# Kernel tuning notes

Hardware: AMD Instinct MI355X
Metric: run time of the kernel (lower is better)

## Reference

```python
import jax, jax.numpy as jnp
import numpy as np

HIDDEN = 4096
NUM_HEADS = 32
HEAD_DIM = 128
NUM_KV_HEADS = 8
KV_GROUPS = NUM_HEADS // NUM_KV_HEADS
ROPE_THETA = 10000.0
SEQ = 2048
BATCH = 1
NEG_INF = -1e9


def fake_quant_int8(x):
    """Per-tensor symmetric int8 fake quantization (absmax scale)."""
    scale = jnp.maximum(jnp.max(jnp.abs(x)) / 127.0, 1e-8)
    q = jnp.clip(jnp.round(x / scale), -127.0, 127.0) * scale
    # straight-through estimator (no-op in fwd-only, keeps code shared)
    return x + jax.lax.stop_gradient(q - x)


def rotate_half(x):
    x1, x2 = jnp.split(x, 2, axis=-1)
    return jnp.concatenate([-x2, x1], axis=-1)


def rope_cos_sin(position_ids):
    inv_freq = 1.0 / (ROPE_THETA ** (jnp.arange(0, HEAD_DIM, 2, dtype=jnp.float32) / HEAD_DIM))
    freqs = position_ids.astype(jnp.float32)[..., None] * inv_freq  # [B,S,HD/2]
    emb = jnp.concatenate([freqs, freqs], axis=-1)                  # [B,S,HD]
    return jnp.cos(emb), jnp.sin(emb)


def setup_inputs() -> dict:
    key = jax.random.key(0)
    k1, k2, k3, k4, k5 = jax.random.split(key, 5)
    hidden_states = jax.random.normal(k1, (BATCH, SEQ, HIDDEN), dtype=jnp.float32)
    causal = jnp.tril(jnp.ones((SEQ, SEQ), dtype=bool))
    attention_mask = jnp.where(causal, 0.0, NEG_INF).astype(jnp.float32)[None, None]  # [1,1,S,S]
    position_ids = jnp.arange(SEQ, dtype=jnp.int64 if jax.config.jax_enable_x64 else jnp.int32)[None, :]
    s = 0.02
    wq = jax.random.normal(k2, (NUM_HEADS * HEAD_DIM, HIDDEN), dtype=jnp.float32) * s
    wk = jax.random.normal(k3, (NUM_KV_HEADS * HEAD_DIM, HIDDEN), dtype=jnp.float32) * s
    wv = jax.random.normal(k4, (NUM_KV_HEADS * HEAD_DIM, HIDDEN), dtype=jnp.float32) * s
    wo = jax.random.normal(k5, (HIDDEN, NUM_HEADS * HEAD_DIM), dtype=jnp.float32) * s
    return {"hidden_states": hidden_states, "attention_mask": attention_mask,
            "position_ids": position_ids, "wq": wq, "wk": wk, "wv": wv, "wo": wo}


def reference(hidden_states, attention_mask, position_ids, wq, wk, wv, wo):
    B, S, _ = hidden_states.shape

    def qlinear(x, w):  # quantized linear: fake-quant act and weight, y = x @ w.T
        return fake_quant_int8(x) @ fake_quant_int8(w).T

    q = qlinear(hidden_states, wq).reshape(B, S, NUM_HEADS, HEAD_DIM).transpose(0, 2, 1, 3)
    k = qlinear(hidden_states, wk).reshape(B, S, NUM_KV_HEADS, HEAD_DIM).transpose(0, 2, 1, 3)
    v = qlinear(hidden_states, wv).reshape(B, S, NUM_KV_HEADS, HEAD_DIM).transpose(0, 2, 1, 3)

    cos, sin = rope_cos_sin(position_ids)      # [B,S,HD]
    cos, sin = cos[:, None], sin[:, None]      # [B,1,S,HD]
    q = q * cos + rotate_half(q) * sin
    k = k * cos + rotate_half(k) * sin

    # repeat_kv: GQA -> full heads
    k = jnp.repeat(k, KV_GROUPS, axis=1)
    v = jnp.repeat(v, KV_GROUPS, axis=1)

    # quantized QK^T
    scores = jnp.einsum('bhqd,bhkd->bhqk', fake_quant_int8(q), fake_quant_int8(k))
    scores = scores * (1.0 / np.sqrt(HEAD_DIM).astype(np.float32))
    scores = scores + attention_mask[:, :, :, :S]
    probs = jax.nn.softmax(scores.astype(jnp.float32), axis=-1).astype(q.dtype)
    # attention_dropout = 0.0 -> identity

    # quantized AV
    attn_out = jnp.einsum('bhqk,bhkd->bhqd', fake_quant_int8(probs), fake_quant_int8(v))
    attn_out = attn_out.transpose(0, 2, 1, 3).reshape(B, S, NUM_HEADS * HEAD_DIM)
    return qlinear(attn_out, wo)
```

## Files before the change

kernel.cpp:

```cpp
#include <hip/hip_runtime.h>
#include <stdint.h>

#define SEQ   2048
#define HID   4096
#define NH    32
#define NKV   8
#define KVDIM 1024
#define KVCAT 2048

typedef int v4i __attribute__((ext_vector_type(4)));

#define VMCNT0 asm volatile("s_waitcnt vmcnt(0)" ::: "memory")

__device__ __forceinline__ void gload16(const void* g, void* l) {
    __builtin_amdgcn_global_load_lds(
        (const __attribute__((address_space(1))) void*)(uintptr_t)g,
        (__attribute__((address_space(3))) void*)(uintptr_t)l, 16, 0, 0);
}

__device__ __forceinline__ float slot_scale(const unsigned* slots, int slot) {
    return fmaxf(__uint_as_float(slots[slot << 5]) / 127.0f, 1e-8f);
}

__device__ __forceinline__ int q8v(float x, float s) {
    int v = (int)rintf(x / s);
    return v < -127 ? -127 : (v > 127 ? 127 : v);
}

__device__ __forceinline__ float fexp2(float x) {
    float r; asm("v_exp_f32 %0, %1" : "=v"(r) : "v"(x)); return r;
}

__device__ __forceinline__ float amax4(const float* __restrict__ p, long v) {
    float4 x = *(const float4*)(p + v * 4);
    return fmaxf(fmaxf(fabsf(x.x), fabsf(x.y)), fmaxf(fabsf(x.z), fabsf(x.w)));
}

__device__ __forceinline__ void block_amax_store(float m, float* part) {
    __shared__ float sm[4];
    int lane = threadIdx.x & 63, w = threadIdx.x >> 6;
    for (int off = 32; off; off >>= 1) m = fmaxf(m, __shfl_xor(m, off, 64));
    if (lane == 0) sm[w] = m;
    __syncthreads();
    if (threadIdx.x == 0)
        part[blockIdx.x] = fmaxf(fmaxf(sm[0], sm[1]), fmaxf(sm[2], sm[3]));
}

#define NV0 ((long)SEQ * HID / 4)
#define NV1 ((long)HID * HID / 4)
#define NV2 ((long)KVDIM * HID / 4)
__global__ void k_absmax5(const float* __restrict__ a0, const float* __restrict__ a1,
                          const float* __restrict__ a2, const float* __restrict__ a3,
                          const float* __restrict__ a4, float* __restrict__ part) {
    int b = blockIdx.x;
    const float* p; long n; int lb, nb;
    if (b < 342)       { p = a0; n = NV0; lb = b;        nb = 342; }
    else if (b < 1025) { p = a1; n = NV1; lb = b - 342;  nb = 683; }
    else if (b < 1196) { p = a2; n = NV2; lb = b - 1025; nb = 171; }
    else if (b < 1367) { p = a3; n = NV2; lb = b - 1196; nb = 171; }
    else               { p = a4; n = NV1; lb = b - 1367; nb = 681; }
    long str = (long)nb * 256;
    float mm[8] = {0.f, 0.f, 0.f, 0.f, 0.f, 0.f, 0.f, 0.f};
    long v = (long)lb * 256 + threadIdx.x;
    for (; v + 7 * str < n; v += 8 * str) {
        #pragma unroll
        for (int j = 0; j < 8; j++) mm[j] = fmaxf(mm[j], amax4(p, v + j * str));
    }
    for (; v < n; v += str) mm[0] = fmaxf(mm[0], amax4(p, v));
    float m = fmaxf(fmaxf(fmaxf(mm[0], mm[1]), fmaxf(mm[2], mm[3])),
                    fmaxf(fmaxf(mm[4], mm[5]), fmaxf(mm[6], mm[7])));
    block_amax_store(m, part);
}

__global__ void k_reduceA(const float* __restrict__ part, unsigned* slots) {
    __shared__ float sm[4];
    const int lo[5] = {0, 342, 1025, 1196, 1367};
    const int hi[5] = {342, 1025, 1196, 1367, 2048};
    int t = threadIdx.x, lane = t & 63, w = t >> 6;
    for (int s = 0; s < 5; s++) {
        float m = 0.f;
        for (int i = lo[s] + t; i < hi[s]; i += 256) m = fmaxf(m, part[i]);
        for (int off = 32; off; off >>= 1) m = fmaxf(m, __shfl_xor(m, off, 64));
        if (lane == 0) sm[w] = m;
        __syncthreads();
        if (t == 0)
            slots[s << 5] = __float_as_uint(fmaxf(fmaxf(sm[0], sm[1]), fmaxf(sm[2], sm[3])));
        __syncthreads();
    }
}

__global__ void k_reduceB(const float* __restrict__ p1, const float* __restrict__ p2,
                          const float* __restrict__ p3, unsigned* slots) {
    __shared__ float sm[4];
    int t = threadIdx.x, lane = t & 63, w = t >> 6;
    const float* ps[3] = {p1, p2, p3};
    const int cnt[3] = {2048, 1024, 256};
    const int sl[3] = {5, 6, 7};
    for (int s = 0; s < 3; s++) {
        float m = 0.f;
        for (int i = t; i < cnt[s]; i += 256) m = fmaxf(m, ps[s][i]);
        for (int off = 32; off; off >>= 1) m = fmaxf(m, __shfl_xor(m, off, 64));
        if (lane == 0) sm[w] = m;
        __syncthreads();
        if (t == 0)
            slots[sl[s] << 5] = __float_as_uint(fmaxf(fmaxf(sm[0], sm[1]), fmaxf(sm[2], sm[3])));
        __syncthreads();
    }
}

__device__ __forceinline__ void qstore4(const float* __restrict__ src, long v,
                                        int8_t* __restrict__ dst, float s) {
    float4 x = *(const float4*)(src + v * 4);
    unsigned pa = (unsigned)(uint8_t)(int8_t)q8v(x.x, s)
                | ((unsigned)(uint8_t)(int8_t)q8v(x.y, s) << 8)
                | ((unsigned)(uint8_t)(int8_t)q8v(x.z, s) << 16)
                | ((unsigned)(uint8_t)(int8_t)q8v(x.w, s) << 24);
    *(unsigned*)(dst + v * 4) = pa;
}

__global__ void k_quant4(const float* __restrict__ a0, const float* __restrict__ a1,
                         const float* __restrict__ a2, const float* __restrict__ a3,
                         int8_t* __restrict__ d0, int8_t* __restrict__ d1,
                         int8_t* __restrict__ d2, int8_t* __restrict__ d3,
                         const unsigned* __restrict__ slots) {
    int b = blockIdx.x;
    const float* p; int8_t* d; long n; int slot, lb, nb;
    if (b < 512)       { p = a0; d = d0; n = NV0; slot = 0; lb = b;        nb = 512; }
    else if (b < 1536) { p = a1; d = d1; n = NV1; slot = 1; lb = b - 512;  nb = 1024; }
    else if (b < 1792) { p = a2; d = d2; n = NV2; slot = 2; lb = b - 1536; nb = 256; }
    else               { p = a3; d = d3; n = NV2; slot = 3; lb = b - 1792; nb = 256; }
    float s = slot_scale(slots, slot);
    long str = (long)nb * 256;
    long v = (long)lb * 256 + threadIdx.x;
    for (; v + 3 * str < n; v += 4 * str) {
        #pragma unroll
        for (int j = 0; j < 4; j++) qstore4(p, v + j * str, d, s);
    }
    for (; v < n; v += str) qstore4(p, v, d, s);
}

__global__ void k_quant(const float* __restrict__ x, int8_t* __restrict__ q, long nvec,
                        int rshift, long cmaskv, long ld,
                        const unsigned* __restrict__ slots, int slot) {
    float s = slot_scale(slots, slot);
    long gs = (long)gridDim.x * blockDim.x;
    long v = blockIdx.x * (long)blockDim.x + threadIdx.x;
    for (; v + 3 * gs < nvec; v += 4 * gs) {
        #pragma unroll
        for (int j = 0; j < 4; j++) {
            long vid = v + j * gs;
            long r = vid >> rshift;
            long c = (vid & cmaskv) << 2;
            float4 vv = *(const float4*)(x + r * ld + c);
            unsigned pa = (unsigned)(uint8_t)(int8_t)q8v(vv.x, s)
                        | ((unsigned)(uint8_t)(int8_t)q8v(vv.y, s) << 8)
                        | ((unsigned)(uint8_t)(int8_t)q8v(vv.z, s) << 16)
                        | ((unsigned)(uint8_t)(int8_t)q8v(vv.w, s) << 24);
            *(unsigned*)(q + vid * 4) = pa;
        }
    }
    for (; v < nvec; v += gs) {
        long r = v >> rshift;
        long c = (v & cmaskv) << 2;
        float4 vv = *(const float4*)(x + r * ld + c);
        unsigned pa = (unsigned)(uint8_t)(int8_t)q8v(vv.x, s)
                    | ((unsigned)(uint8_t)(int8_t)q8v(vv.y, s) << 8)
                    | ((unsigned)(uint8_t)(int8_t)q8v(vv.z, s) << 16)
                    | ((unsigned)(uint8_t)(int8_t)q8v(vv.w, s) << 24);
        *(unsigned*)(q + v * 4) = pa;
    }
}

__global__ void k_ropetab(const int* __restrict__ pos, float* __restrict__ ct,
                          float* __restrict__ st) {
    int tid = blockIdx.x * blockDim.x + threadIdx.x;
    if (tid >= SEQ * 64) return;
    int i = tid & 63, s = tid >> 6;
    double inv = 1.0 / pow(10000.0, (double)((float)(2 * i) * (1.0f / 128.0f)));
    float invf = (float)inv;
    float angf = (float)pos[s] * invf;
    double a = (double)angf;
    ct[tid] = (float)cos(a);
    st[tid] = (float)sin(a);
}

__global__ void k_rope(float* __restrict__ x, long ld, int hbits, int total,
                       const float* __restrict__ ct, const float* __restrict__ st,
                       float* __restrict__ part) {
    float m = 0.f;
    for (int t = blockIdx.x * blockDim.x + threadIdx.x; t < total;
         t += gridDim.x * blockDim.x) {
        int i4 = t & 15;
        int h = (t >> 4) & ((1 << hbits) - 1);
        int s = t >> (4 + hbits);
        long base = (long)s * ld + h * 128 + i4 * 4;
        float4 a = *(float4*)(x + base);
        float4 b = *(float4*)(x + base + 64);
        float4 c = *(const float4*)(ct + s * 64 + i4 * 4);
        float4 sn = *(const float4*)(st + s * 64 + i4 * 4);
        float4 o0, o1;
        o0.x = a.x * c.x - b.x * sn.x;  o1.x = b.x * c.x + a.x * sn.x;
        o0.y = a.y * c.y - b.y * sn.y;  o1.y = b.y * c.y + a.y * sn.y;
        o0.z = a.z * c.z - b.z * sn.z;  o1.z = b.z * c.z + a.z * sn.z;
        o0.w = a.w * c.w - b.w * sn.w;  o1.w = b.w * c.w + a.w * sn.w;
        *(float4*)(x + base) = o0;
        *(float4*)(x + base + 64) = o1;
        m = fmaxf(m,
            fmaxf(fmaxf(fmaxf(fabsf(o0.x), fabsf(o0.y)), fmaxf(fabsf(o0.z), fabsf(o0.w))),
                  fmaxf(fmaxf(fabsf(o1.x), fabsf(o1.y)), fmaxf(fabsf(o1.z), fabsf(o1.w)))));
    }
    block_amax_store(m, part);
}

__global__ void k_transq(const float* __restrict__ src, long lds_, int8_t* __restrict__ dst,
                         long ldd, const unsigned* __restrict__ slots, int slot) {
    __shared__ float t[32][33];
    float s = slot_scale(slots, slot);
    int bx = blockIdx.x, by = blockIdx.y;
    int tid = threadIdx.x;
    int c = tid & 31, r0 = tid >> 5;
    #pragma unroll
    for (int j = 0; j < 4; j++) {
        int r = r0 + j * 8;
        t[r][c] = src[(long)(by * 32 + r) * lds_ + bx * 32 + c];
    }
    __syncthreads();
    int d = tid >> 3, k4 = (tid & 7) * 4;
    unsigned pa = 0;
    #pragma unroll
    for (int j = 0; j < 4; j++) {
        int iv = q8v(t[k4 + j][d], s);
        pa |= ((unsigned)(uint8_t)(int8_t)iv) << (8 * j);
    }
    *(unsigned*)(dst + (long)(bx * 32 + d) * ldd + by * 32 + k4) = pa;
}

__global__ __launch_bounds__(256) void k_gemm_i8(
    const int8_t* __restrict__ A, const int8_t* __restrict__ B, float* __restrict__ C,
    int M, int N, int K, unsigned* slots,
    int slotA, int slotB, int slotB2, int nsplit, float* am_part, int am_col0) {
    __shared__ int8_t As[2][128 * 128];
    __shared__ int8_t Bs[2][128 * 128];
    const v4i vzero = {0, 0, 0, 0};
    int tid = threadIdx.x, lane = tid & 63, wid = tid >> 6;
    int nbx = N >> 7;
    int nwg = gridDim.x, wg = blockIdx.x;
    int cpx = nwg >> 3;
    int swz = (wg & 7) * cpx + (wg >> 3);
    int bm = swz / nbx, bn = swz % nbx;
    long rowA0 = (long)bm * 128, colB0 = (long)bn * 128;
    int wrow = (wid >> 1) * 64, wcol = (wid & 1) * 64;
    int lr = lane >> 3;
    int swc = ((lane & 7) ^ lr) * 16;
    const int8_t* ga = A + (rowA0 + wid * 8 + lr) * (long)K + swc;
    const int8_t* gb = B + (colB0 + wid * 8 + lr) * (long)K + swc;
    v4i acc[4][4];
    #pragma unroll
    for (int m = 0; m < 4; m++)
        #pragma unroll
        for (int n = 0; n < 4; n++) acc[m][n] = vzero;

    auto STAGE = [&](int buf, int kt) {
        #pragma unroll
        for (int i = 0; i < 4; i++) {
            gload16(ga + kt + (long)(i * 32) * K, &As[buf][(wid * 8 + i * 32) * 128]);
            gload16(gb + kt + (long)(i * 32) * K, &Bs[buf][(wid * 8 + i * 32) * 128]);
        }
    };
    auto COMPUTE = [&](int buf) {
        #pragma unroll
        for (int ks = 0; ks < 2; ks++) {
            v4i af[4], bf[4];
            #pragma unroll
            for (int m = 0; m < 4; m++) {
                int row = wrow + m * 16 + (lane & 15);
                af[m] = *(const v4i*)(&As[buf][row * 128 + (((ks * 4 + (lane >> 4)) ^ (row & 7)) * 16)]);
            }
            #pragma unroll
            for (int n = 0; n < 4; n++) {
                int row = wcol + n * 16 + (lane & 15);
                bf[n] = *(const v4i*)(&Bs[buf][row * 128 + (((ks * 4 + (lane >> 4)) ^ (row & 7)) * 16)]);
            }
            #pragma unroll
            for (int m = 0; m < 4; m++)
                #pragma unroll
                for (int n = 0; n < 4; n++)
                    acc[m][n] = __builtin_amdgcn_mfma_i32_16x16x64_i8(af[m], bf[n], acc[m][n], 0, 0, 0);
        }
    };

    STAGE(0, 0);
    VMCNT0;
    __syncthreads();
    int nt = K >> 7, cur = 0;
    for (int t = 0; t < nt - 1; t++) {
        STAGE(cur ^ 1, (t + 1) << 7);
        COMPUTE(cur);
        VMCNT0;
        __syncthreads();
        cur ^= 1;
    }
    COMPUTE(cur);

    float sA = slot_scale(slots, slotA);
    float sB1 = slot_scale(slots, slotB);
    float sB2 = slot_scale(slots, slotB2);
    float am = 0.f;
    #pragma unroll
    for (int m = 0; m < 4; m++) {
        long row0 = rowA0 + wrow + m * 16 + ((lane >> 4) << 2);
        #pragma unroll
        for (int n = 0; n < 4; n++) {
            int col = (int)colB0 + wcol + n * 16 + (lane & 15);
            float sc = sA * ((col < nsplit) ? sB1 : sB2);
            float* cp = C + row0 * N + col;
            #pragma unroll
            for (int r = 0; r < 4; r++) {
                float val = sc * (float)acc[m][n][r];
                cp[(long)r * N] = val;
                if (col >= am_col0) am = fmaxf(am, fabsf(val));
            }
        }
    }
    if (am_part) block_amax_store(am, am_part);
}

__global__ __launch_bounds__(256) void k_attn(
    const int8_t* __restrict__ Qq, const int8_t* __restrict__ Kq, const int8_t* __restrict__ Vtq,
    int* __restrict__ AO, unsigned* slots) {
    __shared__ int8_t Qs[64 * 128];
    __shared__ int8_t Ks[2][64 * 128];
    __shared__ int8_t Vs[2][128 * 64];
    __shared__ int smx[4];
    const v4i vzero = {0, 0, 0, 0};
    const int NEGS = -(1 << 29);
    int tid = threadIdx.x, lane = tid & 63, w = tid >> 6;
    int qlan = lane & 15, g = lane >> 4;
    int idx = blockIdx.x;
    int qb = 31 - (idx >> 5), h = idx & 31, kvh = h >> 2;
    float sq = slot_scale(slots, 5), sk = slot_scale(slots, 6);
    float c2 = sq * sk * 0.08838834764831845f * 1.4426950408889634f;
    int lr8 = lane >> 3;
    int swc = ((lane & 7) ^ lr8) * 16;
    int lr4 = lane >> 2;
    int vswc = ((lane & 3) ^ (lr4 & 3)) * 16;
    const int8_t* kbase = Kq + ((long)(w * 8 + lr8)) * KVDIM + kvh * 128 + swc;
    const int8_t* vbase = Vtq + ((long)kvh * 128 + w * 16 + lr4) * SEQ + vswc;
    auto STAGE_K = [&](int buf, int kt) {
        #pragma unroll
        for (int i = 0; i < 2; i++)
            gload16(kbase + ((long)kt * 64 + i * 32) * KVDIM, &Ks[buf][(w * 8 + i * 32) * 128]);
    };
    auto STAGE_V = [&](int buf, int kt) {
        #pragma unroll
        for (int i = 0; i < 2; i++)
            gload16(vbase + (long)(i * 64) * SEQ + kt * 64, &Vs[buf][(w * 16 + i * 64) * 64]);
    };
    {
        const int8_t* qbase = Qq + ((long)qb * 64 + w * 8 + lr8) * HID + h * 128 + swc;
        #pragma unroll
        for (int i = 0; i < 2; i++)
            gload16(qbase + (long)(i * 32) * HID, &Qs[(w * 8 + i * 32) * 128]);
    }
    STAGE_K(0, 0);
    VMCNT0;
    __syncthreads();
    v4i aq[2];
    #pragma unroll
    for (int ks = 0; ks < 2; ks++) {
        int row = w * 16 + qlan;
        aq[ks] = *(const v4i*)(&Qs[row * 128 + (((ks * 4 + g) ^ (row & 7)) * 16)]);
    }
    int mi = -(1 << 30);
    float l = 0.f;
    int buf = 0;
    for (int kt = 0; kt <= qb; kt++) {
        if (kt < qb) STAGE_K(buf ^ 1, kt + 1);
        v4i sf[4] = {vzero, vzero, vzero, vzero};
        __builtin_amdgcn_s_setprio(1);
        #pragma unroll
        for (int ks = 0; ks < 2; ks++)
            #pragma unroll
            for (int f = 0; f < 4; f++) {
                int row = f * 16 + qlan;
                v4i bk = *(const v4i*)(&Ks[buf][row * 128 + (((ks * 4 + g) ^ (row & 7)) * 16)]);
                sf[f] = __builtin_amdgcn_mfma_i32_16x16x64_i8(bk, aq[ks], sf[f], 0, 0, 0);
            }
        __builtin_amdgcn_s_setprio(0);
        int sv[16];
        if (kt == qb) {
            int qthr = w * 16 + qlan;
            #pragma unroll
            for (int f = 0; f < 4; f++)
                #pragma unroll
                for (int r = 0; r < 4; r++) {
                    int kl = f * 16 + g * 4 + r;
                    sv[f * 4 + r] = (kl > qthr) ? NEGS : sf[f][r];
                }
        } else {
            #pragma unroll
            for (int f = 0; f < 4; f++)
                #pragma unroll
                for (int r = 0; r < 4; r++) sv[f * 4 + r] = sf[f][r];
        }
        int tm = sv[0];
        #pragma unroll
        for (int e = 1; e < 16; e++) tm = tm > sv[e] ? tm : sv[e];
        tm = max(tm, __shfl_xor(tm, 16, 64));
        tm = max(tm, __shfl_xor(tm, 32, 64));
        int mn = tm > mi ? tm : mi;
        float esc = fexp2(c2 * (float)(mi - mn));
        float es = 0.f;
        #pragma unroll
        for (int e = 0; e < 16; e++) es += fexp2(c2 * (float)(sv[e] - mn));
        es += __shfl_xor(es, 16, 64);
        es += __shfl_xor(es, 32, 64);
        l = l * esc + es;
        mi = mn;
        VMCNT0;
        __syncthreads();
        buf ^= 1;
    }
    float invl = 127.0f / l;
    unsigned* Ps32 = (unsigned*)Qs;
    int pwr = w * 320;
    v4i of[8];
    #pragma unroll
    for (int nf = 0; nf < 8; nf++) of[nf] = vzero;
    STAGE_K(0, 0);
    STAGE_V(0, 0);
    VMCNT0;
    __syncthreads();
    buf = 0;
    for (int kt = 0; kt <= qb; kt++) {
        if (kt < qb) { STAGE_K(buf ^ 1, kt + 1); STAGE_V(buf ^ 1, kt + 1); }
        v4i sf[4] = {vzero, vzero, vzero, vzero};
        __builtin_amdgcn_s_setprio(1);
        #pragma unroll
        for (int ks = 0; ks < 2; ks++)
            #pragma unroll
            for (int f = 0; f < 4; f++) {
                int row = f * 16 + qlan;
                v4i bk = *(const v4i*)(&Ks[buf][row * 128 + (((ks * 4 + g) ^ (row & 7)) * 16)]);
                sf[f] = __builtin_amdgcn_mfma_i32_16x16x64_i8(bk, aq[ks], sf[f], 0, 0, 0);
            }
        __builtin_amdgcn_s_setprio(0);
        if (kt == qb) {
            int qthr = w * 16 + qlan;
            #pragma unroll
            for (int f = 0; f < 4; f++) {
                unsigned pk = 0;
                #pragma unroll
                for (int r = 0; r < 4; r++) {
                    int kl = f * 16 + g * 4 + r;
                    int s = (kl > qthr) ? NEGS : sf[f][r];
                    float t = fexp2(c2 * (float)(s - mi));
                    int pq = (int)rintf(t * invl);
                    pk |= ((unsigned)pq) << (8 * r);
                }
                Ps32[pwr + (4 * f + g) * 20 + qlan] = pk;
            }
        } else {
            #pragma unroll
            for (int f = 0; f < 4; f++) {
                unsigned pk = 0;
                #pragma unroll
                for (int r = 0; r < 4; r++) {
                    float t = fexp2(c2 * (float)(sf[f][r] - mi));
                    int pq = (int)rintf(t * invl);
                    pk |= ((unsigned)pq) << (8 * r);
                }
                Ps32[pwr + (4 * f + g) * 20 + qlan] = pk;
            }
        }
        int rb = pwr + 80 * g + qlan;
        v4i ap;
        ap[0] = (int)Ps32[rb];
        ap[1] = (int)Ps32[rb + 20];
        ap[2] = (int)Ps32[rb + 40];
        ap[3] = (int)Ps32[rb + 60];
        __builtin_amdgcn_s_setprio(1);
        #pragma unroll
        for (int nf = 0; nf < 8; nf++) {
            int row = nf * 16 + qlan;
            v4i bv = *(const v4i*)(&Vs[buf][row * 64 + ((g ^ (row & 3)) * 16)]);
            of[nf] = __builtin_amdgcn_mfma_i32_16x16x64_i8(ap, bv, of[nf], 0, 0, 0);
        }
        __builtin_amdgcn_s_setprio(0);
        VMCNT0;
        __syncthreads();
        buf ^= 1;
    }
    int mymax = 0;
    #pragma unroll
    for (int nf = 0; nf < 8; nf++)
        #pragma unroll
        for (int r = 0; r < 4; r++) {
            int val = of[nf][r];
            int av = val < 0 ? -val : val;
            mymax = av > mymax ? av : mymax;
            int qg = qb * 64 + w * 16 + 4 * g + r;
            AO[(long)qg * HID + h * 128 + nf * 16 + qlan] = val;
        }
    #pragma unroll
    for (int off = 1; off < 64; off <<= 1) {
        int o2 = __shfl_xor(mymax, off, 64);
        mymax = o2 > mymax ? o2 : mymax;
    }
    if (lane == 0) smx[w] = mymax;
    __syncthreads();
    if (tid == 0) {
        int mm = max(max(smx[0], smx[1]), max(smx[2], smx[3]));
        atomicMax(slots + (8 << 5), (unsigned)mm);
    }
}

__global__ void k_quant_ao(const int* __restrict__ a, int8_t* __restrict__ q, unsigned* slots) {
    float sv = slot_scale(slots, 7);
    float spv = (1.0f / 127.0f) * sv;
    float amax = spv * (float)(int)slots[8 << 5];
    float s = fmaxf(amax / 127.0f, 1e-8f);
    long nvec = (long)SEQ * HID / 4;
    long gs = (long)gridDim.x * blockDim.x;
    long v = blockIdx.x * (long)blockDim.x + threadIdx.x;
    for (; v + 3 * gs < nvec; v += 4 * gs) {
        #pragma unroll
        for (int j = 0; j < 4; j++) {
            long vid = v + j * gs;
            int4 x = *(const int4*)(a + vid * 4);
            int a0 = q8v(spv * (float)x.x, s);
            int a1 = q8v(spv * (float)x.y, s);
            int a2 = q8v(spv * (float)x.z, s);
            int a3 = q8v(spv * (float)x.w, s);
            unsigned pa = (unsigned)(uint8_t)(int8_t)a0
                        | ((unsigned)(uint8_t)(int8_t)a1 << 8)
                        | ((unsigned)(uint8_t)(int8_t)a2 << 16)
                        | ((unsigned)(uint8_t)(int8_t)a3 << 24);
            *(unsigned*)(q + vid * 4) = pa;
        }
    }
    for (; v < nvec; v += gs) {
        int4 x = *(const int4*)(a + v * 4);
        int a0 = q8v(spv * (float)x.x, s);
        int a1 = q8v(spv * (float)x.y, s);
        int a2 = q8v(spv * (float)x.z, s);
        int a3 = q8v(spv * (float)x.w, s);
        unsigned pa = (unsigned)(uint8_t)(int8_t)a0
                    | ((unsigned)(uint8_t)(int8_t)a1 << 8)
                    | ((unsigned)(uint8_t)(int8_t)a2 << 16)
                    | ((unsigned)(uint8_t)(int8_t)a3 << 24);
        *(unsigned*)(q + v * 4) = pa;
    }
    if (blockIdx.x == 0 && threadIdx.x == 0) slots[9 << 5] = __float_as_uint(amax);
}

extern "C" void kernel_launch(void* const* d_in, const int* in_sizes, int n_in,
                              void* d_out, int out_size, void* d_ws, size_t ws_size,
                              hipStream_t stream) {
    (void)in_sizes; (void)n_in; (void)out_size;
    const float* hid = (const float*)d_in[0];
    const int* pos = (const int*)d_in[2];
    const float* wqp = (const float*)d_in[3];
    const float* wkp = (const float*)d_in[4];
    const float* wvp = (const float*)d_in[5];
    const float* wop = (const float*)d_in[6];
    float* out = (float*)d_out;
    char* ws = (char*)d_ws;

    size_t o = 0;
    auto alloc = [&](size_t sz) { size_t r = o; o += (sz + 255) & ~(size_t)255; return r; };
    unsigned* slots = (unsigned*)(ws + alloc(2048));
    float* P0 = (float*)(ws + alloc(2048 * 4));
    float* P1 = (float*)(ws + alloc(2048 * 4));
    float* P2 = (float*)(ws + alloc(1024 * 4));
    float* P3 = (float*)(ws + alloc(256 * 4));
    int8_t* Xq   = (int8_t*)(ws + alloc((size_t)SEQ * HID));
    int8_t* Wqq  = (int8_t*)(ws + alloc((size_t)HID * HID));
    int8_t* Wkvq = (int8_t*)(ws + alloc((size_t)KVCAT * HID));
    float*  Qf   = (float*)(ws + alloc((size_t)SEQ * HID * 4));
    float*  KVf  = (float*)(ws + alloc((size_t)SEQ * KVCAT * 4));
    int8_t* Qq   = (int8_t*)(ws + alloc((size_t)SEQ * HID));
    int8_t* Kq   = (int8_t*)(ws + alloc((size_t)SEQ * KVDIM));
    int8_t* Vtq  = (int8_t*)(ws + alloc((size_t)KVDIM * SEQ));
    float*  ctab = (float*)(ws + alloc((size_t)SEQ * 64 * 4));
    float*  stab = (float*)(ws + alloc((size_t)SEQ * 64 * 4));
    if (ws_size < o) return;
    int8_t* Woq = Wqq;
    int*    AOint = (int*)Qf;
    int8_t* AOq = Xq;

    hipMemsetAsync(slots, 0, 2048, stream);
    k_ropetab<<<SEQ * 64 / 256, 256, 0, stream>>>(pos, ctab, stab);
    k_absmax5<<<2048, 256, 0, stream>>>(hid, wqp, wkp, wvp, wop, P0);
    k_reduceA<<<1, 256, 0, stream>>>(P0, slots);
    k_quant4<<<2048, 256, 0, stream>>>(hid, wqp, wkp, wvp,
                                       Xq, Wqq, Wkvq, Wkvq + (size_t)KVDIM * HID, slots);
    k_gemm_i8<<<512, 256, 0, stream>>>(Xq, Wqq, Qf, SEQ, HID, HID, slots,
                                       0, 1, 1, 1 << 30, nullptr, 1 << 30);
    k_gemm_i8<<<256, 256, 0, stream>>>(Xq, Wkvq, KVf, SEQ, KVCAT, HID, slots,
                                       0, 2, 3, KVDIM, P3, KVDIM);
    const long CALL = 0x3FFFFFFFL;
    k_quant<<<2048, 256, 0, stream>>>(wop, Woq, (long)HID * HID / 4, 40, CALL, 0, slots, 4);
    k_rope<<<2048, 256, 0, stream>>>(Qf, HID, 5, SEQ * NH * 16, ctab, stab, P1);
    k_rope<<<1024, 256, 0, stream>>>(KVf, KVCAT, 3, SEQ * NKV * 16, ctab, stab, P2);
    k_reduceB<<<1, 256, 0, stream>>>(P1, P2, P3, slots);
    k_quant<<<2048, 256, 0, stream>>>(Qf, Qq, (long)SEQ * HID / 4, 40, CALL, 0, slots, 5);
    k_quant<<<512, 256, 0, stream>>>(KVf, Kq, (long)SEQ * KVDIM / 4, 8, 255, KVCAT, slots, 6);
    k_transq<<<dim3(32, 64), 256, 0, stream>>>(KVf + KVDIM, KVCAT, Vtq, SEQ, slots, 7);
    k_attn<<<1024, 256, 0, stream>>>(Qq, Kq, Vtq, AOint, slots);
    k_quant_ao<<<2048, 256, 0, stream>>>(AOint, AOq, slots);
    k_gemm_i8<<<512, 256, 0, stream>>>(AOq, Woq, out, SEQ, HID, HID, slots,
                                       9, 4, 4, 1 << 30, nullptr, 1 << 30);
}
```

Measured before the change: 312.6 us.

## Fuse RoPE and absmax into GEMM epilogues, add 256x128 GEMM tile, simplify softmax quant

Result: no change. 309.8 us (-0.9%).

```diff
diff --git a/kernel.cpp b/kernel.cpp
--- a/kernel.cpp
+++ b/kernel.cpp
@@ -36,14 +36,30 @@
     return fmaxf(fmaxf(fabsf(x.x), fabsf(x.y)), fmaxf(fabsf(x.z), fabsf(x.w)));
 }
 
-__device__ __forceinline__ void block_amax_store(float m, float* part) {
+__device__ __forceinline__ void block_amax_part(float m, float* dst) {
     __shared__ float sm[4];
     int lane = threadIdx.x & 63, w = threadIdx.x >> 6;
     for (int off = 32; off; off >>= 1) m = fmaxf(m, __shfl_xor(m, off, 64));
     if (lane == 0) sm[w] = m;
     __syncthreads();
     if (threadIdx.x == 0)
-        part[blockIdx.x] = fmaxf(fmaxf(sm[0], sm[1]), fmaxf(sm[2], sm[3]));
+        *dst = fmaxf(fmaxf(sm[0], sm[1]), fmaxf(sm[2], sm[3]));
+    __syncthreads();
+}
+
+__device__ __forceinline__ void block_amax_part8(float m, float* dst) {
+    __shared__ float sm8[8];
+    int lane = threadIdx.x & 63, w = threadIdx.x >> 6;
+    for (int off = 32; off; off >>= 1) m = fmaxf(m, __shfl_xor(m, off, 64));
+    if (lane == 0) sm8[w] = m;
+    __syncthreads();
+    if (threadIdx.x == 0) {
+        float r = sm8[0];
+        #pragma unroll
+        for (int i = 1; i < 8; i++) r = fmaxf(r, sm8[i]);
+        *dst = r;
+    }
+    __syncthreads();
 }
 
 #define NV0 ((long)SEQ * HID / 4)
@@ -69,7 +85,7 @@
     for (; v < n; v += str) mm[0] = fmaxf(mm[0], amax4(p, v));
     float m = fmaxf(fmaxf(fmaxf(mm[0], mm[1]), fmaxf(mm[2], mm[3])),
                     fmaxf(fmaxf(mm[4], mm[5]), fmaxf(mm[6], mm[7])));
-    block_amax_store(m, part);
+    block_amax_part(m, part + blockIdx.x);
 }
 
 __global__ void k_reduceA(const float* __restrict__ part, unsigned* slots) {
@@ -94,7 +110,7 @@
     __shared__ float sm[4];
     int t = threadIdx.x, lane = t & 63, w = t >> 6;
     const float* ps[3] = {p1, p2, p3};
-    const int cnt[3] = {2048, 1024, 256};
+    const int cnt[3] = {256, 128, 128};
     const int sl[3] = {5, 6, 7};
     for (int s = 0; s < 3; s++) {
         float m = 0.f;
@@ -184,34 +200,6 @@
     st[tid] = (float)sin(a);
 }
 
-__global__ void k_rope(float* __restrict__ x, long ld, int hbits, int total,
-                       const float* __restrict__ ct, const float* __restrict__ st,
-                       float* __restrict__ part) {
-    float m = 0.f;
-    for (int t = blockIdx.x * blockDim.x + threadIdx.x; t < total;
-         t += gridDim.x * blockDim.x) {
-        int i4 = t & 15;
-        int h = (t >> 4) & ((1 << hbits) - 1);
-        int s = t >> (4 + hbits);
-        long base = (long)s * ld + h * 128 + i4 * 4;
-        float4 a = *(float4*)(x + base);
-        float4 b = *(float4*)(x + base + 64);
-        float4 c = *(const float4*)(ct + s * 64 + i4 * 4);
-        float4 sn = *(const float4*)(st + s * 64 + i4 * 4);
-        float4 o0, o1;
-        o0.x = a.x * c.x - b.x * sn.x;  o1.x = b.x * c.x + a.x * sn.x;
-        o0.y = a.y * c.y - b.y * sn.y;  o1.y = b.y * c.y + a.y * sn.y;
-        o0.z = a.z * c.z - b.z * sn.z;  o1.z = b.z * c.z + a.z * sn.z;
-        o0.w = a.w * c.w - b.w * sn.w;  o1.w = b.w * c.w + a.w * sn.w;
-        *(float4*)(x + base) = o0;
-        *(float4*)(x + base + 64) = o1;
-        m = fmaxf(m,
-            fmaxf(fmaxf(fmaxf(fabsf(o0.x), fabsf(o0.y)), fmaxf(fabsf(o0.z), fabsf(o0.w))),
-                  fmaxf(fmaxf(fabsf(o1.x), fabsf(o1.y)), fmaxf(fabsf(o1.z), fabsf(o1.w)))));
-    }
-    block_amax_store(m, part);
-}
-
 __global__ void k_transq(const float* __restrict__ src, long lds_, int8_t* __restrict__ dst,
                          long ldd, const unsigned* __restrict__ slots, int slot) {
     __shared__ float t[32][33];
@@ -238,9 +226,12 @@
 __global__ __launch_bounds__(256) void k_gemm_i8(
     const int8_t* __restrict__ A, const int8_t* __restrict__ B, float* __restrict__ C,
     int M, int N, int K, unsigned* slots,
-    int slotA, int slotB, int slotB2, int nsplit, float* am_part, int am_col0) {
-    __shared__ int8_t As[2][128 * 128];
-    __shared__ int8_t Bs[2][128 * 128];
+    int slotA, int slotB, int slotB2, int nsplit,
+    float* pK, float* pV,
+    const float* __restrict__ ct, const float* __restrict__ st) {
+    __shared__ int8_t POOL[65536];
+    int8_t (*As)[16384] = (int8_t(*)[16384])POOL;
+    int8_t (*Bs)[16384] = (int8_t(*)[16384])(POOL + 32768);
     const v4i vzero = {0, 0, 0, 0};
     int tid = threadIdx.x, lane = tid & 63, wid = tid >> 6;
     int nbx = N >> 7;
@@ -305,24 +296,195 @@
     float sA = slot_scale(slots, slotA);
     float sB1 = slot_scale(slots, slotB);
     float sB2 = slot_scale(slots, slotB2);
-    float am = 0.f;
+    int qc = lane & 15, rgrp = (lane >> 4) << 2;
+    if (bn < 8) {
+        __syncthreads();
+        float* EX = (float*)POOL;
+        #pragma unroll
+        for (int m = 0; m < 4; m++)
+            #pragma unroll
+            for (int n = 0; n < 4; n++) {
+                int coll = wcol + n * 16 + qc;
+                #pragma unroll
+                for (int r = 0; r < 4; r++) {
+                    int rowl = wrow + m * 16 + rgrp + r;
+                    EX[rowl * 128 + (coll ^ ((rowl & 1) << 4))] = sA * sB1 * (float)acc[m][n][r];
+                }
+            }
+        __syncthreads();
+        float am = 0.f;
+        #pragma unroll
+        for (int m = 0; m < 4; m++)
+            #pragma unroll
+            for (int n = 0; n < 4; n++) {
+                int coll = wcol + n * 16 + qc;
+                #pragma unroll
+                for (int r = 0; r < 4; r++) {
+                    int rowl = wrow + m * 16 + rgrp + r;
+                    long srow = rowA0 + rowl;
+                    float self = EX[rowl * 128 + (coll ^ ((rowl & 1) << 4))];
+                    float pv = EX[rowl * 128 + ((coll ^ 64) ^ ((rowl & 1) << 4))];
+                    float c = ct[srow * 64 + (coll & 63)];
+                    float sn = st[srow * 64 + (coll & 63)];
+                    float o = (coll < 64) ? self * c - pv * sn : self * c + pv * sn;
+                    am = fmaxf(am, fabsf(o));
+                    C[srow * N + colB0 + coll] = o;
+                }
+            }
+        block_amax_part(am, pK + bm * 8 + (bn & 7));
+    } else {
+        float am = 0.f;
+        #pragma unroll
+        for (int m = 0; m < 4; m++) {
+            long row0 = rowA0 + wrow + m * 16 + rgrp;
+            #pragma unroll
+            for (int n = 0; n < 4; n++) {
+                int col = (int)colB0 + wcol + n * 16 + qc;
+                float sc = sA * ((col < nsplit) ? sB1 : sB2);
+                float* cp = C + row0 * N + col;
+                #pragma unroll
+                for (int r = 0; r < 4; r++) {
+                    float val = sc * (float)acc[m][n][r];
+                    cp[(long)r * N] = val;
+                    am = fmaxf(am, fabsf(val));
+                }
+            }
+        }
+        block_amax_part(am, pV + bm * 8 + (bn & 7));
+    }
+}
+
+__global__ __launch_bounds__(512) void k_gemm_big(
+    const int8_t* __restrict__ A, const int8_t* __restrict__ B, float* __restrict__ C,
+    int N, int K, unsigned* slots, int slotA, int slotB,
+    float* pQ, int do_rope,
+    const float* __restrict__ ct, const float* __restrict__ st) {
+    __shared__ int8_t POOL[98304];
+    int8_t (*As)[32768] = (int8_t(*)[32768])POOL;
+    int8_t (*Bs)[16384] = (int8_t(*)[16384])(POOL + 65536);
+    const v4i vzero = {0, 0, 0, 0};
+    int tid = threadIdx.x, lane = tid & 63, wid = tid >> 6;
+    int nbx = N >> 7;
+    int nwg = gridDim.x, wg = blockIdx.x;
+    int cpx = nwg >> 3;
+    int swz = (wg & 7) * cpx + (wg >> 3);
+    int bm = swz / nbx, bn = swz % nbx;
+    long rowA0 = (long)bm * 256, colB0 = (long)bn * 128;
+    int wrow = (wid >> 1) * 64, wcol = (wid & 1) * 64;
+    int lr = lane >> 3;
+    int swc = ((lane & 7) ^ lr) * 16;
+    const int8_t* ga = A + (rowA0 + wid * 8 + lr) * (long)K + swc;
+    const int8_t* gb = B + (colB0 + wid * 8 + lr) * (long)K + swc;
+    v4i acc[4][4];
     #pragma unroll
-    for (int m = 0; m < 4; m++) {
-        long row0 = rowA0 + wrow + m * 16 + ((lane >> 4) << 2);
-        #pragma unroll
-        for (int n = 0; n < 4; n++) {
-            int col = (int)colB0 + wcol + n * 16 + (lane & 15);
-            float sc = sA * ((col < nsplit) ? sB1 : sB2);
-            float* cp = C + row0 * N + col;
-            #pragma unroll
-            for (int r = 0; r < 4; r++) {
-                float val = sc * (float)acc[m][n][r];
-                cp[(long)r * N] = val;
-                if (col >= am_col0) am = fmaxf(am, fabsf(val));
-            }
-        }
-    }
-    if (am_part) block_amax_store(am, am_part);
+    for (int m = 0; m < 4; m++)
+        #pragma unroll
+        for (int n = 0; n < 4; n++) acc[m][n] = vzero;
+
+    auto STAGE = [&](int buf, int kt) {
+        #pragma unroll
+        for (int i = 0; i < 4; i++)
+            gload16(ga + kt + (long)(i * 64) * K, &As[buf][(wid * 8 + i * 64) * 128]);
+        #pragma unroll
+        for (int i = 0; i < 2; i++)
+            gload16(gb + kt + (long)(i * 64) * K, &Bs[buf][(wid * 8 + i * 64) * 128]);
+    };
+    auto COMPUTE = [&](int buf) {
+        #pragma unroll
+        for (int ks = 0; ks < 2; ks++) {
+            v4i af[4], bf[4];
+            #pragma unroll
+            for (int m = 0; m < 4; m++) {
+                int row = wrow + m * 16 + (lane & 15);
+                af[m] = *(const v4i*)(&As[buf][row * 128 + (((ks * 4 + (lane >> 4)) ^ (row & 7)) * 16)]);
+            }
+            #pragma unroll
+            for (int n = 0; n < 4; n++) {
+                int row = wcol + n * 16 + (lane & 15);
+                bf[n] = *(const v4i*)(&Bs[buf][row * 128 + (((ks * 4 + (lane >> 4)) ^ (row & 7)) * 16)]);
+            }
+            #pragma unroll
+            for (int m = 0; m < 4; m++)
+                #pragma unroll
+                for (int n = 0; n < 4; n++)
+                    acc[m][n] = __builtin_amdgcn_mfma_i32_16x16x64_i8(af[m], bf[n], acc[m][n], 0, 0, 0);
+        }
+    };
+
+    STAGE(0, 0);
+    VMCNT0;
+    __syncthreads();
+    int nt = K >> 7, cur = 0;
+    for (int t = 0; t < nt - 1; t++) {
+        STAGE(cur ^ 1, (t + 1) << 7);
+        COMPUTE(cur);
+        VMCNT0;
+        __syncthreads();
+        cur ^= 1;
+    }
+    COMPUTE(cur);
+
+    float sA = slot_scale(slots, slotA);
+    float sB1 = slot_scale(slots, slotB);
+    int qc = lane & 15, rgrp = (lane >> 4) << 2;
+    if (do_rope) {
+        float am = 0.f;
+        float* EX = (float*)POOL;
+        __syncthreads();
+        #pragma unroll
+        for (int half = 0; half < 2; half++) {
+            if ((wid >> 2) == half) {
+                #pragma unroll
+                for (int m = 0; m < 4; m++)
+                    #pragma unroll
+                    for (int n = 0; n < 4; n++) {
+                        int coll = wcol + n * 16 + qc;
+                        #pragma unroll
+                        for (int r = 0; r < 4; r++) {
+                            int exr = wrow + m * 16 + rgrp + r - half * 128;
+                            EX[exr * 128 + (coll ^ (((exr >> 2) & 3) << 4))] =
+                                sA * sB1 * (float)acc[m][n][r];
+                        }
+                    }
+            }
+            __syncthreads();
+            if ((wid >> 2) == half) {
+                #pragma unroll
+                for (int m = 0; m < 4; m++)
+                    #pragma unroll
+                    for (int n = 0; n < 4; n++) {
+                        int coll = wcol + n * 16 + qc;
+                        #pragma unroll
+                        for (int r = 0; r < 4; r++) {
+                            int exr = wrow + m * 16 + rgrp + r - half * 128;
+                            int xm = ((exr >> 2) & 3) << 4;
+                            float self = EX[exr * 128 + (coll ^ xm)];
+                            float pv = EX[exr * 128 + ((coll ^ 64) ^ xm)];
+                            long srow = rowA0 + half * 128 + exr;
+                            float c = ct[srow * 64 + (coll & 63)];
+                            float sn = st[srow * 64 + (coll & 63)];
+                            float o = (coll < 64) ? self * c - pv * sn : self * c + pv * sn;
+                            am = fmaxf(am, fabsf(o));
+                            C[srow * N + colB0 + coll] = o;
+                        }
+                    }
+            }
+            __syncthreads();
+        }
+        block_amax_part8(am, pQ + blockIdx.x);
+    } else {
+        #pragma unroll
+        for (int m = 0; m < 4; m++) {
+            long row0 = rowA0 + wrow + m * 16 + rgrp;
+            #pragma unroll
+            for (int n = 0; n < 4; n++) {
+                int col = (int)colB0 + wcol + n * 16 + qc;
+                float* cp = C + row0 * N + col;
+                #pragma unroll
+                for (int r = 0; r < 4; r++) cp[(long)r * N] = sA * sB1 * (float)acc[m][n][r];
+            }
+        }
+    }
 }
 
 __global__ __launch_bounds__(256) void k_attn(
@@ -334,6 +496,7 @@
     __shared__ int smx[4];
     const v4i vzero = {0, 0, 0, 0};
     const int NEGS = -(1 << 29);
+    const float MAGIC = 12582912.0f;
     int tid = threadIdx.x, lane = tid & 63, w = tid >> 6;
     int qlan = lane & 15, g = lane >> 4;
     int idx = blockIdx.x;
@@ -409,10 +572,12 @@
         tm = max(tm, __shfl_xor(tm, 16, 64));
         tm = max(tm, __shfl_xor(tm, 32, 64));
         int mn = tm > mi ? tm : mi;
-        float esc = fexp2(c2 * (float)(mi - mn));
+        float fm = (float)mn;
+        float nb = -c2 * fm;
+        float esc = fexp2(fmaf((float)mi, c2, nb));
         float es = 0.f;
         #pragma unroll
-        for (int e = 0; e < 16; e++) es += fexp2(c2 * (float)(sv[e] - mn));
+        for (int e = 0; e < 16; e++) es += fexp2(fmaf((float)sv[e], c2, nb));
         es += __shfl_xor(es, 16, 64);
         es += __shfl_xor(es, 32, 64);
         l = l * esc + es;
@@ -421,7 +586,7 @@
         __syncthreads();
         buf ^= 1;
     }
-    float invl = 127.0f / l;
+    float Bq = fmaf(c2, (float)mi, __log2f(l) - 6.9886846867721655f);
     unsigned* Ps32 = (unsigned*)Qs;
     int pwr = w * 320;
     v4i of[8];
@@ -454,9 +619,9 @@
                 for (int r = 0; r < 4; r++) {
                     int kl = f * 16 + g * 4 + r;
                     int s = (kl > qthr) ? NEGS : sf[f][r];
-                    float t = fexp2(c2 * (float)(s - mi));
-                    int pq = (int)rintf(t * invl);
-                    pk |= ((unsigned)pq) << (8 * r);
+                    float t = fexp2(fmaf((float)s, c2, -Bq));
+                    unsigned u = __float_as_uint(t + MAGIC) & 127u;
+                    pk |= u << (8 * r);
                 }
                 Ps32[pwr + (4 * f + g) * 20 + qlan] = pk;
             }
@@ -466,9 +631,9 @@
                 unsigned pk = 0;
                 #pragma unroll
                 for (int r = 0; r < 4; r++) {
-                    float t = fexp2(c2 * (float)(sf[f][r] - mi));
-                    int pq = (int)rintf(t * invl);
-                    pk |= ((unsigned)pq) << (8 * r);
+                    float t = fexp2(fmaf((float)sf[f][r], c2, -Bq));
+                    unsigned u = __float_as_uint(t + MAGIC) & 127u;
+                    pk |= u << (8 * r);
                 }
                 Ps32[pwr + (4 * f + g) * 20 + qlan] = pk;
             }
@@ -571,9 +736,9 @@
     auto alloc = [&](size_t sz) { size_t r = o; o += (sz + 255) & ~(size_t)255; return r; };
     unsigned* slots = (unsigned*)(ws + alloc(2048));
     float* P0 = (float*)(ws + alloc(2048 * 4));
-    float* P1 = (float*)(ws + alloc(2048 * 4));
-    float* P2 = (float*)(ws + alloc(1024 * 4));
-    float* P3 = (float*)(ws + alloc(256 * 4));
+    float* P1 = (float*)(ws + alloc(256 * 4));
+    float* P2 = (float*)(ws + alloc(128 * 4));
+    float* P3 = (float*)(ws + alloc(128 * 4));
     int8_t* Xq   = (int8_t*)(ws + alloc((size_t)SEQ * HID));
     int8_t* Wqq  = (int8_t*)(ws + alloc((size_t)HID * HID));
     int8_t* Wkvq = (int8_t*)(ws + alloc((size_t)KVCAT * HID));
@@ -595,20 +760,18 @@
     k_reduceA<<<1, 256, 0, stream>>>(P0, slots);
     k_quant4<<<2048, 256, 0, stream>>>(hid, wqp, wkp, wvp,
                                        Xq, Wqq, Wkvq, Wkvq + (size_t)KVDIM * HID, slots);
-    k_gemm_i8<<<512, 256, 0, stream>>>(Xq, Wqq, Qf, SEQ, HID, HID, slots,
-                                       0, 1, 1, 1 << 30, nullptr, 1 << 30);
+    k_gemm_big<<<256, 512, 0, stream>>>(Xq, Wqq, Qf, HID, HID, slots,
+                                        0, 1, P1, 1, ctab, stab);
     k_gemm_i8<<<256, 256, 0, stream>>>(Xq, Wkvq, KVf, SEQ, KVCAT, HID, slots,
-                                       0, 2, 3, KVDIM, P3, KVDIM);
+                                       0, 2, 3, KVDIM, P2, P3, ctab, stab);
     const long CALL = 0x3FFFFFFFL;
     k_quant<<<2048, 256, 0, stream>>>(wop, Woq, (long)HID * HID / 4, 40, CALL, 0, slots, 4);
-    k_rope<<<2048, 256, 0, stream>>>(Qf, HID, 5, SEQ * NH * 16, ctab, stab, P1);
-    k_rope<<<1024, 256, 0, stream>>>(KVf, KVCAT, 3, SEQ * NKV * 16, ctab, stab, P2);
     k_reduceB<<<1, 256, 0, stream>>>(P1, P2, P3, slots);
     k_quant<<<2048, 256, 0, stream>>>(Qf, Qq, (long)SEQ * HID / 4, 40, CALL, 0, slots, 5);
     k_quant<<<512, 256, 0, stream>>>(KVf, Kq, (long)SEQ * KVDIM / 4, 8, 255, KVCAT, slots, 6);
     k_transq<<<dim3(32, 64), 256, 0, stream>>>(KVf + KVDIM, KVCAT, Vtq, SEQ, slots, 7);
     k_attn<<<1024, 256, 0, stream>>>(Qq, Kq, Vtq, AOint, slots);
     k_quant_ao<<<2048, 256, 0, stream>>>(AOint, AOq, slots);
-    k_gemm_i8<<<512, 256, 0, stream>>>(AOq, Woq, out, SEQ, HID, HID, slots,
-                                       9, 4, 4, 1 << 30, nullptr, 1 << 30);
-}
+    k_gemm_big<<<256, 512, 0, stream>>>(AOq, Woq, out, HID, HID, slots,
+                                        9, 4, nullptr, 0, nullptr, nullptr);
+}
```

## Fuse RoPE and absmax into int8 GEMM epilogue; cheapen softmax quantization

Applied to the files above, without the earlier changes.

After: 301.0 us. -3.7%, faster.

```diff
diff --git a/kernel.cpp b/kernel.cpp
--- a/kernel.cpp
+++ b/kernel.cpp
@@ -36,14 +36,15 @@
     return fmaxf(fmaxf(fabsf(x.x), fabsf(x.y)), fmaxf(fabsf(x.z), fabsf(x.w)));
 }
 
-__device__ __forceinline__ void block_amax_store(float m, float* part) {
+__device__ __forceinline__ void block_amax_part(float m, float* dst) {
     __shared__ float sm[4];
     int lane = threadIdx.x & 63, w = threadIdx.x >> 6;
     for (int off = 32; off; off >>= 1) m = fmaxf(m, __shfl_xor(m, off, 64));
     if (lane == 0) sm[w] = m;
     __syncthreads();
     if (threadIdx.x == 0)
-        part[blockIdx.x] = fmaxf(fmaxf(sm[0], sm[1]), fmaxf(sm[2], sm[3]));
+        *dst = fmaxf(fmaxf(sm[0], sm[1]), fmaxf(sm[2], sm[3]));
+    __syncthreads();
 }
 
 #define NV0 ((long)SEQ * HID / 4)
@@ -69,7 +70,7 @@
     for (; v < n; v += str) mm[0] = fmaxf(mm[0], amax4(p, v));
     float m = fmaxf(fmaxf(fmaxf(mm[0], mm[1]), fmaxf(mm[2], mm[3])),
                     fmaxf(fmaxf(mm[4], mm[5]), fmaxf(mm[6], mm[7])));
-    block_amax_store(m, part);
+    block_amax_part(m, part + blockIdx.x);
 }
 
 __global__ void k_reduceA(const float* __restrict__ part, unsigned* slots) {
@@ -94,7 +95,7 @@
     __shared__ float sm[4];
     int t = threadIdx.x, lane = t & 63, w = t >> 6;
     const float* ps[3] = {p1, p2, p3};
-    const int cnt[3] = {2048, 1024, 256};
+    const int cnt[3] = {512, 128, 128};
     const int sl[3] = {5, 6, 7};
     for (int s = 0; s < 3; s++) {
         float m = 0.f;
@@ -184,34 +185,6 @@
     st[tid] = (float)sin(a);
 }
 
-__global__ void k_rope(float* __restrict__ x, long ld, int hbits, int total,
-                       const float* __restrict__ ct, const float* __restrict__ st,
-                       float* __restrict__ part) {
-    float m = 0.f;
-    for (int t = blockIdx.x * blockDim.x + threadIdx.x; t < total;
-         t += gridDim.x * blockDim.x) {
-        int i4 = t & 15;
-        int h = (t >> 4) & ((1 << hbits) - 1);
-        int s = t >> (4 + hbits);
-        long base = (long)s * ld + h * 128 + i4 * 4;
-        float4 a = *(float4*)(x + base);
-        float4 b = *(float4*)(x + base + 64);
-        float4 c = *(const float4*)(ct + s * 64 + i4 * 4);
-        float4 sn = *(const float4*)(st + s * 64 + i4 * 4);
-        float4 o0, o1;
-        o0.x = a.x * c.x - b.x * sn.x;  o1.x = b.x * c.x + a.x * sn.x;
-        o0.y = a.y * c.y - b.y * sn.y;  o1.y = b.y * c.y + a.y * sn.y;
-        o0.z = a.z * c.z - b.z * sn.z;  o1.z = b.z * c.z + a.z * sn.z;
-        o0.w = a.w * c.w - b.w * sn.w;  o1.w = b.w * c.w + a.w * sn.w;
-        *(float4*)(x + base) = o0;
-        *(float4*)(x + base + 64) = o1;
-        m = fmaxf(m,
-            fmaxf(fmaxf(fmaxf(fabsf(o0.x), fabsf(o0.y)), fmaxf(fabsf(o0.z), fabsf(o0.w))),
-                  fmaxf(fmaxf(fabsf(o1.x), fabsf(o1.y)), fmaxf(fabsf(o1.z), fabsf(o1.w)))));
-    }
-    block_amax_store(m, part);
-}
-
 __global__ void k_transq(const float* __restrict__ src, long lds_, int8_t* __restrict__ dst,
                          long ldd, const unsigned* __restrict__ slots, int slot) {
     __shared__ float t[32][33];
@@ -238,9 +211,12 @@
 __global__ __launch_bounds__(256) void k_gemm_i8(
     const int8_t* __restrict__ A, const int8_t* __restrict__ B, float* __restrict__ C,
     int M, int N, int K, unsigned* slots,
-    int slotA, int slotB, int slotB2, int nsplit, float* am_part, int am_col0) {
-    __shared__ int8_t As[2][128 * 128];
-    __shared__ int8_t Bs[2][128 * 128];
+    int slotA, int slotB, int slotB2, int nsplit,
+    float* pQ, float* pK, float* pV, int ropemode,
+    const float* __restrict__ ct, const float* __restrict__ st) {
+    __shared__ int8_t POOL[65536];
+    int8_t (*As)[16384] = (int8_t(*)[16384])POOL;
+    int8_t (*Bs)[16384] = (int8_t(*)[16384])(POOL + 32768);
     const v4i vzero = {0, 0, 0, 0};
     int tid = threadIdx.x, lane = tid & 63, wid = tid >> 6;
     int nbx = N >> 7;
@@ -305,24 +281,75 @@
     float sA = slot_scale(slots, slotA);
     float sB1 = slot_scale(slots, slotB);
     float sB2 = slot_scale(slots, slotB2);
-    float am = 0.f;
-    #pragma unroll
-    for (int m = 0; m < 4; m++) {
-        long row0 = rowA0 + wrow + m * 16 + ((lane >> 4) << 2);
-        #pragma unroll
-        for (int n = 0; n < 4; n++) {
-            int col = (int)colB0 + wcol + n * 16 + (lane & 15);
-            float sc = sA * ((col < nsplit) ? sB1 : sB2);
-            float* cp = C + row0 * N + col;
-            #pragma unroll
-            for (int r = 0; r < 4; r++) {
-                float val = sc * (float)acc[m][n][r];
-                cp[(long)r * N] = val;
-                if (col >= am_col0) am = fmaxf(am, fabsf(val));
-            }
-        }
-    }
-    if (am_part) block_amax_store(am, am_part);
+    int qc = lane & 15, rgrp = (lane >> 4) << 2;
+    if (ropemode == 1 || (ropemode == 2 && bn < 8)) {
+        __syncthreads();
+        float* EX = (float*)POOL;
+        #pragma unroll
+        for (int m = 0; m < 4; m++)
+            #pragma unroll
+            for (int n = 0; n < 4; n++) {
+                int coll = wcol + n * 16 + qc;
+                #pragma unroll
+                for (int r = 0; r < 4; r++) {
+                    int rowl = wrow + m * 16 + rgrp + r;
+                    EX[rowl * 128 + (coll ^ ((rowl & 1) << 4))] = sA * sB1 * (float)acc[m][n][r];
+                }
+            }
+        __syncthreads();
+        float am = 0.f;
+        #pragma unroll
+        for (int m = 0; m < 4; m++)
+            #pragma unroll
+            for (int n = 0; n < 4; n++) {
+                int coll = wcol + n * 16 + qc;
+                #pragma unroll
+                for (int r = 0; r < 4; r++) {
+                    int rowl = wrow + m * 16 + rgrp + r;
+                    long srow = rowA0 + rowl;
+                    float self = EX[rowl * 128 + (coll ^ ((rowl & 1) << 4))];
+                    float pv = EX[rowl * 128 + ((coll ^ 64) ^ ((rowl & 1) << 4))];
+                    float c = ct[srow * 64 + (coll & 63)];
+                    float sn = st[srow * 64 + (coll & 63)];
+                    float o = (coll < 64) ? self * c - pv * sn : self * c + pv * sn;
+                    am = fmaxf(am, fabsf(o));
+                    C[srow * N + colB0 + coll] = o;
+                }
+            }
+        block_amax_part(am, (ropemode == 1) ? pQ + blockIdx.x : pK + bm * 8 + (bn & 7));
+    } else if (ropemode == 2) {
+        float am = 0.f;
+        #pragma unroll
+        for (int m = 0; m < 4; m++) {
+            long row0 = rowA0 + wrow + m * 16 + rgrp;
+            #pragma unroll
+            for (int n = 0; n < 4; n++) {
+                int col = (int)colB0 + wcol + n * 16 + qc;
+                float sc = sA * ((col < nsplit) ? sB1 : sB2);
+                float* cp = C + row0 * N + col;
+                #pragma unroll
+                for (int r = 0; r < 4; r++) {
+                    float val = sc * (float)acc[m][n][r];
+                    cp[(long)r * N] = val;
+                    am = fmaxf(am, fabsf(val));
+                }
+            }
+        }
+        block_amax_part(am, pV + bm * 8 + (bn & 7));
+    } else {
+        #pragma unroll
+        for (int m = 0; m < 4; m++) {
+            long row0 = rowA0 + wrow + m * 16 + rgrp;
+            #pragma unroll
+            for (int n = 0; n < 4; n++) {
+                int col = (int)colB0 + wcol + n * 16 + qc;
+                float sc = sA * ((col < nsplit) ? sB1 : sB2);
+                float* cp = C + row0 * N + col;
+                #pragma unroll
+                for (int r = 0; r < 4; r++) cp[(long)r * N] = sc * (float)acc[m][n][r];
+            }
+        }
+    }
 }
 
 __global__ __launch_bounds__(256) void k_attn(
@@ -334,6 +361,7 @@
     __shared__ int smx[4];
     const v4i vzero = {0, 0, 0, 0};
     const int NEGS = -(1 << 29);
+    const float MAGIC = 12582912.0f;
     int tid = threadIdx.x, lane = tid & 63, w = tid >> 6;
     int qlan = lane & 15, g = lane >> 4;
     int idx = blockIdx.x;
@@ -409,10 +437,11 @@
         tm = max(tm, __shfl_xor(tm, 16, 64));
         tm = max(tm, __shfl_xor(tm, 32, 64));
         int mn = tm > mi ? tm : mi;
-        float esc = fexp2(c2 * (float)(mi - mn));
+        float nb = -c2 * (float)mn;
+        float esc = fexp2(fmaf((float)mi, c2, nb));
         float es = 0.f;
         #pragma unroll
-        for (int e = 0; e < 16; e++) es += fexp2(c2 * (float)(sv[e] - mn));
+        for (int e = 0; e < 16; e++) es += fexp2(fmaf((float)sv[e], c2, nb));
         es += __shfl_xor(es, 16, 64);
         es += __shfl_xor(es, 32, 64);
         l = l * esc + es;
@@ -421,7 +450,7 @@
         __syncthreads();
         buf ^= 1;
     }
-    float invl = 127.0f / l;
+    float Bq = fmaf(c2, (float)mi, __log2f(l) - 6.9886846867721655f);
     unsigned* Ps32 = (unsigned*)Qs;
     int pwr = w * 320;
     v4i of[8];
@@ -454,9 +483,9 @@
                 for (int r = 0; r < 4; r++) {
                     int kl = f * 16 + g * 4 + r;
                     int s = (kl > qthr) ? NEGS : sf[f][r];
-                    float t = fexp2(c2 * (float)(s - mi));
-                    int pq = (int)rintf(t * invl);
-                    pk |= ((unsigned)pq) << (8 * r);
+                    float t = fexp2(fmaf((float)s, c2, -Bq));
+                    unsigned u = __float_as_uint(t + MAGIC) & 127u;
+                    pk |= u << (8 * r);
                 }
                 Ps32[pwr + (4 * f + g) * 20 + qlan] = pk;
             }
@@ -466,9 +495,9 @@
                 unsigned pk = 0;
                 #pragma unroll
                 for (int r = 0; r < 4; r++) {
-                    float t = fexp2(c2 * (float)(sf[f][r] - mi));
-                    int pq = (int)rintf(t * invl);
-                    pk |= ((unsigned)pq) << (8 * r);
+                    float t = fexp2(fmaf((float)sf[f][r], c2, -Bq));
+                    unsigned u = __float_as_uint(t + MAGIC) & 127u;
+                    pk |= u << (8 * r);
                 }
                 Ps32[pwr + (4 * f + g) * 20 + qlan] = pk;
             }
@@ -571,9 +600,9 @@
     auto alloc = [&](size_t sz) { size_t r = o; o += (sz + 255) & ~(size_t)255; return r; };
     unsigned* slots = (unsigned*)(ws + alloc(2048));
     float* P0 = (float*)(ws + alloc(2048 * 4));
-    float* P1 = (float*)(ws + alloc(2048 * 4));
-    float* P2 = (float*)(ws + alloc(1024 * 4));
-    float* P3 = (float*)(ws + alloc(256 * 4));
+    float* P1 = (float*)(ws + alloc(512 * 4));
+    float* P2 = (float*)(ws + alloc(128 * 4));
+    float* P3 = (float*)(ws + alloc(128 * 4));
     int8_t* Xq   = (int8_t*)(ws + alloc((size_t)SEQ * HID));
     int8_t* Wqq  = (int8_t*)(ws + alloc((size_t)HID * HID));
     int8_t* Wkvq = (int8_t*)(ws + alloc((size_t)KVCAT * HID));
@@ -596,13 +625,11 @@
     k_quant4<<<2048, 256, 0, stream>>>(hid, wqp, wkp, wvp,
                                        Xq, Wqq, Wkvq, Wkvq + (size_t)KVDIM * HID, slots);
     k_gemm_i8<<<512, 256, 0, stream>>>(Xq, Wqq, Qf, SEQ, HID, HID, slots,
-                                       0, 1, 1, 1 << 30, nullptr, 1 << 30);
+                                       0, 1, 1, 1 << 30, P1, nullptr, nullptr, 1, ctab, stab);
     k_gemm_i8<<<256, 256, 0, stream>>>(Xq, Wkvq, KVf, SEQ, KVCAT, HID, slots,
-                                       0, 2, 3, KVDIM, P3, KVDIM);
+                                       0, 2, 3, KVDIM, nullptr, P2, P3, 2, ctab, stab);
     const long CALL = 0x3FFFFFFFL;
     k_quant<<<2048, 256, 0, stream>>>(wop, Woq, (long)HID * HID / 4, 40, CALL, 0, slots, 4);
-    k_rope<<<2048, 256, 0, stream>>>(Qf, HID, 5, SEQ * NH * 16, ctab, stab, P1);
-    k_rope<<<1024, 256, 0, stream>>>(KVf, KVCAT, 3, SEQ * NKV * 16, ctab, stab, P2);
     k_reduceB<<<1, 256, 0, stream>>>(P1, P2, P3, slots);
     k_quant<<<2048, 256, 0, stream>>>(Qf, Qq, (long)SEQ * HID / 4, 40, CALL, 0, slots, 5);
     k_quant<<<512, 256, 0, stream>>>(KVf, Kq, (long)SEQ * KVDIM / 4, 8, 255, KVCAT, slots, 6);
@@ -610,5 +637,6 @@
     k_attn<<<1024, 256, 0, stream>>>(Qq, Kq, Vtq, AOint, slots);
     k_quant_ao<<<2048, 256, 0, stream>>>(AOint, AOq, slots);
     k_gemm_i8<<<512, 256, 0, stream>>>(AOq, Woq, out, SEQ, HID, HID, slots,
-                                       9, 4, 4, 1 << 30, nullptr, 1 << 30);
-}
+                                       9, 4, 4, 1 << 30, nullptr, nullptr, nullptr, 0,
+                                       nullptr, nullptr);
+}
```
